# Kernel optimization log

Measured on AMD Instinct MI355X. Metric: run time of the kernel, lower is better.

Reference implementation:

```python
import jax, jax.numpy as jnp
import numpy as np

B = 65536
X_DIM = 362
A = 3  # action_space / number of expert dynamics MLPs


def setup_inputs() -> dict:
    key = jax.random.key(0)
    ks = jax.random.split(key, 12)
    batch_x = jax.random.normal(ks[0], (B, X_DIM), dtype=jnp.float32)
    batch_next = jax.random.normal(ks[1], (B, X_DIM), dtype=jnp.float32)
    # Plant the pointer sentinel (value 10.0) at a random in-bounds grid cell per row,
    # so that ptr-19 >= 0 and ptr+19 < X_DIM (grid width is 19).
    ptr_pos = jax.random.randint(ks[2], (B,), 20, 343)
    batch_x = batch_x.at[jnp.arange(B), ptr_pos].set(10.0)
    batch_a = jax.random.randint(ks[3], (B,), 0, A, dtype=jnp.int32)

    def lin(k, fan_in, shape):
        return (jax.random.normal(k, shape, dtype=jnp.float32) / np.sqrt(fan_in)).astype(jnp.float32)

    W1 = lin(ks[4], 6, (A, 6, 100));   b1 = jnp.zeros((A, 100), jnp.float32)
    W2 = lin(ks[5], 100, (A, 100, 400)); b2 = jnp.zeros((A, 400), jnp.float32)
    W3 = lin(ks[6], 400, (A, 400, 100)); b3 = jnp.zeros((A, 100), jnp.float32)
    W4 = lin(ks[7], 100, (A, 100, 6));  b4 = jnp.zeros((A, 6), jnp.float32)
    return {"batch_x": batch_x, "batch_next": batch_next, "batch_a": batch_a,
            "W1": W1, "b1": b1, "W2": W2, "b2": b2, "W3": W3, "b3": b3, "W4": W4, "b4": b4}


def _attend(data, ptr):
    # cell_list = [0, p, p-19 (left), p+19 (right), p-1 (above), p+1 (below)]
    zeros = jnp.zeros_like(ptr)
    idx = jnp.stack([zeros, ptr, ptr - 19, ptr + 19, ptr - 1, ptr + 1], axis=1)  # [B, 6]
    return jnp.take_along_axis(data, idx, axis=1)  # [B, 6]


def _expert(x, a, W1, b1, W2, b2, W3, b3, W4, b4):
    h = jax.nn.relu(x @ W1[a] + b1[a])
    h = jax.nn.relu(h @ W2[a] + b2[a])
    h = jax.nn.relu(h @ W3[a] + b3[a])
    return h @ W4[a] + b4[a]


def reference(batch_x, batch_next, batch_a, W1, b1, W2, b2, W3, b3, W4, b4):
    # Pointer index = first occurrence of sentinel value 10.0 per row.
    ptr = jnp.argmax(batch_x == 10.0, axis=1)  # [B]
    att = _attend(batch_x, ptr)        # [B, 6]
    att_next = _attend(batch_next, ptr)  # [B, 6]
    # Per-action routed expert MLPs (A is small and fixed): compute each expert
    # over the batch and select per-sample by action id.
    preds = jnp.zeros_like(att)
    for a in range(A):
        out_a = _expert(att, a, W1, b1, W2, b2, W3, b3, W4, b4)
        preds = jnp.where((batch_a == a)[:, None], out_a, preds)
    actual_deltas = att_next - att
    return jnp.mean((preds - actual_deltas) ** 2)
```

## Files before the change

kernel.cpp:

```cpp
#include <hip/hip_runtime.h>
#include <hip/hip_bf16.h>

#define B_ROWS 65536
#define XD 362

typedef __bf16 bf16;
typedef __attribute__((ext_vector_type(8))) __bf16 bf16x8;
typedef __attribute__((ext_vector_type(4))) float f32x4;
typedef __attribute__((ext_vector_type(2))) float f32x2;

#define MFMA16(A, Bf, C) __builtin_amdgcn_mfma_f32_16x16x32_bf16(A, Bf, C, 0, 0, 0)
#define ORDER() __builtin_amdgcn_sched_barrier(0x7F)

#define OFF_W1T   0u
#define OFF_W2T   21504u
#define OFF_W3T   340992u
#define OFF_W4T   620544u
#define OFF_CNT   632832u
#define OFF_PTR   633088u
#define OFF_ATTC  895232u
#define OFF_DELTA 4040960u
#define OFF_PART  8759552u

#define MLP_GRID 520
#define WPREP_BLOCKS 624
#define SCAN_BLOCKS 2896


__global__ __launch_bounds__(256) void k_prep(
    const float* __restrict__ W1, const float* __restrict__ b1,
    const float* __restrict__ W2, const float* __restrict__ b2,
    const float* __restrict__ W3, const float* __restrict__ b3,
    const float* __restrict__ W4, const float* __restrict__ b4,
    const float* __restrict__ x,
    bf16* __restrict__ W1t, bf16* __restrict__ W2t,
    bf16* __restrict__ W3t, bf16* __restrict__ W4t,
    int* __restrict__ cnt, int* __restrict__ ptrArr)
{
  int bx = blockIdx.x;
  if (bx >= WPREP_BLOCKS) {
    int gid = (bx - WPREP_BLOCKS) * 256 + threadIdx.x;
    const float4* x4 = (const float4*)x;
#pragma unroll
    for (int u = 0; u < 8; ++u) {
      int i = gid + u * (SCAN_BLOCKS * 256);
      float4 v = x4[i];
      if (v.x == 10.0f || v.y == 10.0f || v.z == 10.0f || v.w == 10.0f) {
        int flat = i * 4;
        if (v.x == 10.0f) ptrArr[(flat    ) / XD] = (flat    ) % XD;
        if (v.y == 10.0f) ptrArr[(flat + 1) / XD] = (flat + 1) % XD;
        if (v.z == 10.0f) ptrArr[(flat + 2) / XD] = (flat + 2) % XD;
        if (v.w == 10.0f) ptrArr[(flat + 3) / XD] = (flat + 3) % XD;
      }
    }
    return;
  }
  int i = bx * 256 + threadIdx.x;
  if (i == 0) { cnt[0] = 0; cnt[1] = 0; cnt[2] = 0; }
  if (i < 3*416*128) {
    int e = i & 7; int g = (i >> 3) & 15;
    int rn = i >> 7; int n = rn % 416; int a = rn / 416;
    int k = ((g ^ (n & 7)) << 3) | e;
    float v = 0.f;
    if (n < 400) {
      if (k < 100) v = W2[(a*100 + k)*400 + n];
      else if (k == 100) v = b2[a*400 + n];
    } else if (n == 400) {
      v = (k == 100) ? 1.0f : 0.0f;
    }
    W2t[i] = (bf16)v;
  }
  if (i < 3*13*112*32) {
    int e = i & 7; int g = (i >> 3) & 3;
    int n = (i >> 5) % 112; int tc = ((i >> 5) / 112) % 13; int a = i / (13*112*32);
    int k = tc * 32 + ((g ^ (n & 3)) << 3) + e;
    float v = 0.f;
    if (n < 100) {
      if (k < 400) v = W3[(a*400 + k)*100 + n];
      else if (k == 400) v = b3[a*100 + n];
    }
    W3t[i] = (bf16)v;
  }
  if (i < 3*112*32) {
    int k = i & 31; int rn = i >> 5; int n = rn % 112; int a = rn / 112;
    float v = 0.f;
    if (n < 100) {
      if (k < 6) v = W1[(a*6 + k)*100 + n];
      else if (k == 6) v = b1[a*100 + n];
    }
    W1t[i] = (bf16)v;
  }
  if (i < 3*16*128) {
    int k = i & 127; int rn = i >> 7; int n = rn & 15; int a = rn >> 4;
    float v = 0.f;
    if (n < 6) {
      if (k < 100) v = W4[(a*100 + k)*6 + n];
      else if (k == 100) v = b4[a*6 + n];
    }
    W4t[i] = (bf16)v;
  }
}

__global__ __launch_bounds__(256) void k_gather2(
    const float* __restrict__ x, const float* __restrict__ xn,
    const int* __restrict__ act, const int* __restrict__ ptrArr,
    bf16* __restrict__ attC, float* __restrict__ deltaC, int* __restrict__ cnt)
{
  int row = blockIdx.x * 256 + threadIdx.x;
  int lane = threadIdx.x & 63;
  int p = ptrArr[row];
  if (p < 20 || p > 342) p = 20;
  const float* xr = x  + (size_t)row * XD;
  const float* nr = xn + (size_t)row * XD;
  int cells[6] = {0, p, p - 19, p + 19, p - 1, p + 1};
  float av[6], dv[6];
#pragma unroll
  for (int i = 0; i < 6; ++i) {
    av[i] = xr[cells[i]];
    dv[i] = nr[cells[i]] - av[i];
  }
  int a = act[row];
  unsigned long long m0 = __ballot(a == 0);
  unsigned long long m1 = __ballot(a == 1);
  unsigned long long m2 = __ballot(a == 2);
  int b0 = 0, b1 = 0, b2 = 0;
  if (lane == 0) {
    b0 = atomicAdd(&cnt[0], (int)__popcll(m0));
    b1 = atomicAdd(&cnt[1], (int)__popcll(m1));
    b2 = atomicAdd(&cnt[2], (int)__popcll(m2));
  }
  b0 = __shfl(b0, 0); b1 = __shfl(b1, 0); b2 = __shfl(b2, 0);
  unsigned long long lt = (1ull << lane) - 1ull;
  unsigned long long ma = (a == 0) ? m0 : (a == 1) ? m1 : m2;
  int base            = (a == 0) ? b0 : (a == 1) ? b1 : b2;
  int slot = base + (int)__popcll(ma & lt);
  size_t rb = (size_t)a * B_ROWS + slot;
  bf16x8 av8;
#pragma unroll
  for (int i = 0; i < 6; ++i) av8[i] = (bf16)av[i];
  av8[6] = (bf16)1.0f;
  av8[7] = (bf16)0.0f;
  *(bf16x8*)(attC + rb * 8) = av8;
  f32x2 d01 = {dv[0], dv[1]}, d23 = {dv[2], dv[3]}, d45 = {dv[4], dv[5]};
  *(f32x2*)(deltaC + rb * 6)     = d01;
  *(f32x2*)(deltaC + rb * 6 + 2) = d23;
  *(f32x2*)(deltaC + rb * 6 + 4) = d45;
}

__global__ __launch_bounds__(256, 2) void k_mlp(
    const bf16* __restrict__ W1t, const bf16* __restrict__ W2t,
    const bf16* __restrict__ W3t, const bf16* __restrict__ W4t,
    const bf16* __restrict__ attC, const float* __restrict__ deltaC,
    const int* __restrict__ cnt, float* __restrict__ partial)
{
  int c0 = cnt[0], c1 = cnt[1], c2 = cnt[2];
  int T0 = (c0 + 127) >> 7, T1 = (c1 + 127) >> 7, T2 = (c2 + 127) >> 7;
  int b = blockIdx.x;
  int a, tile, count;
  if (b < T0)           { a = 0; tile = b;            count = c0; }
  else if (b < T0 + T1) { a = 1; tile = b - T0;       count = c1; }
  else if (b < T0 + T1 + T2) { a = 2; tile = b - T0 - T1; count = c2; }
  else { if (threadIdx.x == 0) partial[b] = 0.f; return; }
  int start = tile << 7;

  __shared__ __align__(16) bf16 bufW2[2][32][128];
  __shared__ __align__(16) bf16 bufW3[2][112][32];
  __shared__ __align__(16) bf16 h1s[4][16][136];
  __shared__ __align__(16) bf16 tr[4][2][16][56];
  __shared__ float s_part[4];
  int wv = threadIdx.x >> 6, lane = threadIdx.x & 63;
  int q = lane >> 4, c = lane & 15;
  int cx7 = c & 7, cx3 = c & 3;

  const bf16* W1a = W1t + a * 112 * 32;
  const bf16* W2a = W2t + a * 416 * 128;
  const bf16* W3a = W3t + a * 13 * 112 * 32;
  const bf16* W4a = W4t + a * 16 * 128;

  auto stage = [&](int tn) {
    const char* s2 = (const char*)W2a + tn * 8192;
    const char* s3 = (const char*)W3a + tn * 7168;
    char* d2 = (char*)&bufW2[tn & 1][0][0];
    char* d3 = (char*)&bufW3[tn & 1][0][0];
#pragma unroll
    for (int id = wv; id < 15; id += 4) {
      const char* src = (id < 8) ? s2 + id * 1024 + lane * 16
                                 : s3 + (id - 8) * 1024 + lane * 16;
      char* dst = (id < 8) ? d2 + id * 1024 : d3 + (id - 8) * 1024;
      __builtin_amdgcn_global_load_lds(
          (const __attribute__((address_space(1))) unsigned int*)src,
          (__attribute__((address_space(3))) unsigned int*)dst, 16, 0, 0);
    }
  };

  stage(0);

  for (int i = lane; i < 16 * 16; i += 64)
    h1s[wv][i >> 4][112 + (i & 15)] = (bf16)0.0f;

  bf16x8 A2[2][4];
#pragma unroll
  for (int mi = 0; mi < 2; ++mi) {
    bf16x8 aAtt;
#pragma unroll
    for (int i = 0; i < 8; ++i) aAtt[i] = (bf16)0.0f;
    int slot = start + wv * 32 + mi * 16 + c;
    if (q == 0 && slot < count)
      aAtt = *(const bf16x8*)(attC + ((size_t)a * B_ROWS + slot) * 8);
#pragma unroll
    for (int nt = 0; nt < 7; ++nt) {
      bf16x8 bw = *(const bf16x8*)(W1a + (nt * 16 + c) * 32 + q * 8);
      f32x4 C = {0.f, 0.f, 0.f, 0.f};
      C = MFMA16(aAtt, bw, C);
      int n = nt * 16 + c;
#pragma unroll
      for (int rg = 0; rg < 4; ++rg) {
        float v = (n < 100) ? (C[rg] > 0.f ? C[rg] : 0.f)
                            : (n == 100 ? 1.0f : 0.0f);
        h1s[wv][q * 4 + rg][n] = (bf16)v;
      }
    }
    ORDER();
#pragma unroll
    for (int tt = 0; tt < 4; ++tt)
      A2[mi][tt] = *(const bf16x8*)&h1s[wv][c][tt * 32 + q * 8];
    ORDER();
  }

  f32x4 C3[2][7];
#pragma unroll
  for (int mi = 0; mi < 2; ++mi)
#pragma unroll
    for (int i = 0; i < 7; ++i) C3[mi][i] = (f32x4){0.f, 0.f, 0.f, 0.f};

  __syncthreads();

#pragma unroll 1
  for (int t = 0; t < 13; ++t) {
    if (t < 12) stage(t + 1);
    __builtin_amdgcn_sched_barrier(0);

    const bf16* cw2 = &bufW2[t & 1][0][0];
    const bf16* cw3 = &bufW3[t & 1][0][0];
    bf16x8 w3f[7];
#pragma unroll
    for (int nt3 = 0; nt3 < 7; ++nt3)
      w3f[nt3] = *(const bf16x8*)(cw3 + (nt3 * 16 + c) * 32 + ((q ^ cx3) << 3));
    bf16x8 b2f[2][4];
#pragma unroll
    for (int half = 0; half < 2; ++half)
#pragma unroll
      for (int tt = 0; tt < 4; ++tt)
        b2f[half][tt] = *(const bf16x8*)(cw2 + (half * 16 + c) * 128 +
                                         ((((tt << 2) + q) ^ cx7) << 3));

#pragma unroll
    for (int mi = 0; mi < 2; ++mi)
#pragma unroll
      for (int half = 0; half < 2; ++half) {
        f32x4 C = {0.f, 0.f, 0.f, 0.f};
#pragma unroll
        for (int tt = 0; tt < 4; ++tt)
          C = MFMA16(A2[mi][tt], b2f[half][tt], C);
#pragma unroll
        for (int rg = 0; rg < 4; ++rg) {
          float v = C[rg] > 0.f ? C[rg] : 0.f;
          tr[wv][mi][q * 4 + rg][half * 16 + c] = (bf16)v;
        }
      }
    ORDER();
    bf16x8 A3a = *(const bf16x8*)&tr[wv][0][c][q * 8];
    bf16x8 A3b = *(const bf16x8*)&tr[wv][1][c][q * 8];
#pragma unroll
    for (int nt3 = 0; nt3 < 7; ++nt3) {
      C3[0][nt3] = MFMA16(A3a, w3f[nt3], C3[0][nt3]);
      C3[1][nt3] = MFMA16(A3b, w3f[nt3], C3[1][nt3]);
    }
    ORDER();
    __syncthreads();
  }

  bf16x8 b4f[4];
#pragma unroll
  for (int tt = 0; tt < 4; ++tt)
    b4f[tt] = *(const bf16x8*)(W4a + c * 128 + tt * 32 + q * 8);
  float sq = 0.f;
#pragma unroll
  for (int mi = 0; mi < 2; ++mi) {
#pragma unroll
    for (int nt3 = 0; nt3 < 7; ++nt3) {
      int n = nt3 * 16 + c;
#pragma unroll
      for (int rg = 0; rg < 4; ++rg) {
        float v = (n < 100) ? (C3[mi][nt3][rg] > 0.f ? C3[mi][nt3][rg] : 0.f)
                            : (n == 100 ? 1.0f : 0.0f);
        h1s[wv][q * 4 + rg][n] = (bf16)v;
      }
    }
    ORDER();
    f32x4 C4 = {0.f, 0.f, 0.f, 0.f};
#pragma unroll
    for (int tt = 0; tt < 4; ++tt) {
      bf16x8 A4 = *(const bf16x8*)&h1s[wv][c][tt * 32 + q * 8];
      C4 = MFMA16(A4, b4f[tt], C4);
    }
    ORDER();
    if (c < 6) {
#pragma unroll
      for (int rg = 0; rg < 4; ++rg) {
        int slot = start + wv * 32 + mi * 16 + q * 4 + rg;
        if (slot < count) {
          float d = deltaC[((size_t)a * B_ROWS + slot) * 6 + c];
          float e = C4[rg] - d;
          sq += e * e;
        }
      }
    }
  }
#pragma unroll
  for (int off = 32; off; off >>= 1) sq += __shfl_xor(sq, off);
  if (lane == 0) s_part[wv] = sq;
  __syncthreads();
  if (threadIdx.x == 0)
    partial[b] = s_part[0] + s_part[1] + s_part[2] + s_part[3];
}

__global__ __launch_bounds__(256) void k_final(
    const float* __restrict__ partial, float* __restrict__ out)
{
  __shared__ float s[4];
  int t = threadIdx.x, lane = t & 63, wv = t >> 6;
  float sum = 0.f;
  for (int i = t; i < MLP_GRID; i += 256) sum += partial[i];
#pragma unroll
  for (int off = 32; off; off >>= 1) sum += __shfl_xor(sum, off);
  if (lane == 0) s[wv] = sum;
  __syncthreads();
  if (t == 0) {
    double tot = (double)s[0] + s[1] + s[2] + s[3];
    out[0] = (float)(tot / (double)(B_ROWS * 6));
  }
}

extern "C" void kernel_launch(void* const* d_in, const int* in_sizes, int n_in,
                              void* d_out, int out_size, void* d_ws, size_t ws_size,
                              hipStream_t stream)
{
  const float* x  = (const float*)d_in[0];
  const float* xn = (const float*)d_in[1];
  const int*  act = (const int*)d_in[2];
  const float* W1 = (const float*)d_in[3];
  const float* b1 = (const float*)d_in[4];
  const float* W2 = (const float*)d_in[5];
  const float* b2 = (const float*)d_in[6];
  const float* W3 = (const float*)d_in[7];
  const float* b3 = (const float*)d_in[8];
  const float* W4 = (const float*)d_in[9];
  const float* b4 = (const float*)d_in[10];

  char* ws = (char*)d_ws;
  bf16*   W1t    = (bf16*)(ws + OFF_W1T);
  bf16*   W2t    = (bf16*)(ws + OFF_W2T);
  bf16*   W3t    = (bf16*)(ws + OFF_W3T);
  bf16*   W4t    = (bf16*)(ws + OFF_W4T);
  int*    cnt    = (int*)(ws + OFF_CNT);
  int*    ptrArr = (int*)(ws + OFF_PTR);
  bf16*   attC   = (bf16*)(ws + OFF_ATTC);
  float*  deltaC = (float*)(ws + OFF_DELTA);
  float*  part   = (float*)(ws + OFF_PART);

  k_prep<<<dim3(WPREP_BLOCKS + SCAN_BLOCKS), dim3(256), 0, stream>>>(
      W1, b1, W2, b2, W3, b3, W4, b4, x, W1t, W2t, W3t, W4t, cnt, ptrArr);
  k_gather2<<<dim3(B_ROWS / 256), dim3(256), 0, stream>>>(x, xn, act, ptrArr,
                                                          attC, deltaC, cnt);
  k_mlp<<<dim3(MLP_GRID), dim3(256), 0, stream>>>(W1t, W2t, W3t, W4t,
                                                  attC, deltaC, cnt, part);
  k_final<<<dim3(1), dim3(256), 0, stream>>>(part, (float*)d_out);
}
```

Baseline: 272.9 us.

## Triple-buffer W2/W3 LDS staging with counted vmcnt waits and single barrier

Moves the W2/W3 LDS staging from a double buffer to a triple buffer. Each wave now issues exactly four global_load_lds per stage, using a dummy LDS slot so the count is uniform. Instead of a full __syncthreads at the end of each iteration, waves wait with vmcnt(4) so only the previous stage must have landed, then hit one s_barrier. This lets the next tile's loads stay in flight across the barrier and removes one barrier per iteration. The cost is more LDS per block, which could reduce occupancy, and the correctness now depends on hand-counted waitcnt values.

```diff
diff --git a/kernel.cpp b/kernel.cpp
--- a/kernel.cpp
+++ b/kernel.cpp
@@ -163,8 +163,9 @@
   else { if (threadIdx.x == 0) partial[b] = 0.f; return; }
   int start = tile << 7;
 
-  __shared__ __align__(16) bf16 bufW2[2][32][128];
-  __shared__ __align__(16) bf16 bufW3[2][112][32];
+  __shared__ __align__(16) bf16 bufW2[3][32][128];
+  __shared__ __align__(16) bf16 bufW3[3][112][32];
+  __shared__ __align__(16) bf16 dummyLds[512];
   __shared__ __align__(16) bf16 h1s[4][16][136];
   __shared__ __align__(16) bf16 tr[4][2][16][56];
   __shared__ float s_part[4];
@@ -178,15 +179,19 @@
   const bf16* W4a = W4t + a * 16 * 128;
 
   auto stage = [&](int tn) {
+    int sl = tn % 3;
     const char* s2 = (const char*)W2a + tn * 8192;
     const char* s3 = (const char*)W3a + tn * 7168;
-    char* d2 = (char*)&bufW2[tn & 1][0][0];
-    char* d3 = (char*)&bufW3[tn & 1][0][0];
-#pragma unroll
-    for (int id = wv; id < 15; id += 4) {
-      const char* src = (id < 8) ? s2 + id * 1024 + lane * 16
-                                 : s3 + (id - 8) * 1024 + lane * 16;
-      char* dst = (id < 8) ? d2 + id * 1024 : d3 + (id - 8) * 1024;
+    char* d2 = (char*)&bufW2[sl][0][0];
+    char* d3 = (char*)&bufW3[sl][0][0];
+#pragma unroll
+    for (int r = 0; r < 4; ++r) {
+      int id = wv + r * 4;
+      const char* src;
+      char* dst;
+      if (id < 8)       { src = s2 + id * 1024 + lane * 16;       dst = d2 + id * 1024; }
+      else if (id < 15) { src = s3 + (id - 8) * 1024 + lane * 16; dst = d3 + (id - 8) * 1024; }
+      else              { src = s3 + 6 * 1024 + lane * 16;        dst = (char*)&dummyLds[0]; }
       __builtin_amdgcn_global_load_lds(
           (const __attribute__((address_space(1))) unsigned int*)src,
           (__attribute__((address_space(3))) unsigned int*)dst, 16, 0, 0);
@@ -233,15 +238,20 @@
 #pragma unroll
     for (int i = 0; i < 7; ++i) C3[mi][i] = (f32x4){0.f, 0.f, 0.f, 0.f};
 
-  __syncthreads();
-
 #pragma unroll 1
   for (int t = 0; t < 13; ++t) {
-    if (t < 12) stage(t + 1);
+    if (t < 12) {
+      stage(t + 1);
+      asm volatile("s_waitcnt vmcnt(4)" ::: "memory");
+    } else {
+      asm volatile("s_waitcnt vmcnt(0)" ::: "memory");
+    }
+    __builtin_amdgcn_s_barrier();
     __builtin_amdgcn_sched_barrier(0);
 
-    const bf16* cw2 = &bufW2[t & 1][0][0];
-    const bf16* cw3 = &bufW3[t & 1][0][0];
+    int sl = t % 3;
+    const bf16* cw2 = &bufW2[sl][0][0];
+    const bf16* cw3 = &bufW3[sl][0][0];
     bf16x8 w3f[7];
 #pragma unroll
     for (int nt3 = 0; nt3 < 7; ++nt3)
@@ -277,7 +287,8 @@
       C3[1][nt3] = MFMA16(A3b, w3f[nt3], C3[1][nt3]);
     }
     ORDER();
-    __syncthreads();
+    asm volatile("s_waitcnt lgkmcnt(0)" ::: "memory");
+    __builtin_amdgcn_sched_barrier(0);
   }
 
   bf16x8 b4f[4];
```

New measurement: 272.7 us. About the same (-0.1%).
